# Optimization experiments

Measured on AMD Instinct MI355X. Metric: run time of the kernel, lower is better.

## Reference

```python
import jax, jax.numpy as jnp
import numpy as np

NUM_GROUPS = 32
EPS = 1e-6


def group_norm(x, gamma, beta):
    # x: [B, C, H, W]
    b, c, h, w = x.shape
    xg = x.reshape(b, NUM_GROUPS, c // NUM_GROUPS, h, w)
    mean = xg.mean(axis=(2, 3, 4), keepdims=True)
    var = xg.var(axis=(2, 3, 4), keepdims=True)
    xn = ((xg - mean) * jax.lax.rsqrt(var + EPS)).reshape(b, c, h, w)
    return xn * gamma[None, :, None, None] + beta[None, :, None, None]


def setup_inputs() -> dict:
    key = jax.random.key(0)
    ks = jax.random.split(key, 10)
    B, C, H, W = 2, 512, 64, 64
    s = 1.0 / np.sqrt(C)
    return {
        "x": jax.random.normal(ks[0], (B, C, H, W), dtype=jnp.float32),
        "gamma": jnp.ones((C,), jnp.float32),
        "beta": jnp.zeros((C,), jnp.float32),
        "Wq": jax.random.normal(ks[1], (C, C), jnp.float32) * s,
        "bq": jnp.zeros((C,), jnp.float32),
        "Wk": jax.random.normal(ks[2], (C, C), jnp.float32) * s,
        "bk": jnp.zeros((C,), jnp.float32),
        "Wv": jax.random.normal(ks[3], (C, C), jnp.float32) * s,
        "bv": jnp.zeros((C,), jnp.float32),
        "Wo": jax.random.normal(ks[4], (C, C), jnp.float32) * s,
        "bo": jnp.zeros((C,), jnp.float32),
    }


def reference(x, gamma, beta, Wq, bq, Wk, bk, Wv, bv, Wo, bo):
    b, c, h, w = x.shape
    hn = group_norm(x, gamma, beta)               # [B,C,H,W]
    hf = hn.reshape(b, c, h * w)                  # [B,C,N]
    # 1x1 convs == channel matmuls
    q = jnp.einsum('oc,bcn->bon', Wq, hf) + bq[None, :, None]
    k = jnp.einsum('oc,bcn->bon', Wk, hf) + bk[None, :, None]
    v = jnp.einsum('oc,bcn->bon', Wv, hf) + bv[None, :, None]
    scale = float(c) ** -0.5
    scores = jnp.einsum('bci,bcj->bij', q, k) * scale   # [B,N,N]
    attn = jax.nn.softmax(scores, axis=-1)
    out = jnp.einsum('bij,bcj->bci', attn, v)            # [B,C,N]
    out = jnp.einsum('oc,bcn->bon', Wo, out) + bo[None, :, None]
    return x + out.reshape(b, c, h, w)
```

## Files before the change

### kernel.cpp

```cpp
#include <hip/hip_runtime.h>

#define BB 2
#define CC 512
#define NS 4096
#define NGROUP 32
#define TILE 128
#define RSTRIDE 132

typedef __bf16 bf16_8 __attribute__((ext_vector_type(8)));
typedef __bf16 bf16_4 __attribute__((ext_vector_type(4)));
typedef float f32_4 __attribute__((ext_vector_type(4)));

#define SMEM_BYTES 65536
#define SMEM256 131072

__device__ __forceinline__ void gld_lds16(const __bf16* g, __bf16* l) {
  __builtin_amdgcn_global_load_lds(
      (const __attribute__((address_space(1))) unsigned int*)g,
      (__attribute__((address_space(3))) unsigned int*)l, 16, 0, 0);
}

__global__ __launch_bounds__(256) void prep(const float* __restrict__ w0, const float* __restrict__ w1,
                                            const float* __restrict__ w2, const float* __restrict__ w3,
                                            __bf16* __restrict__ o0, __bf16* __restrict__ o1,
                                            __bf16* __restrict__ o2, __bf16* __restrict__ o3,
                                            const float* __restrict__ x,
                                            float* __restrict__ st) {
  const int bid = blockIdx.x;
  if (bid >= 1024) {
    const int idx = bid - 1024;
    const int g = idx >> 2;
    const int ch = idx & 3;
    const float4* p = (const float4*)(x + (size_t)g * 65536 + (size_t)ch * 16384);
    float s = 0.f, q = 0.f;
    for (int i = threadIdx.x; i < 4096; i += 256) {
      float4 v = p[i];
      s += v.x + v.y + v.z + v.w;
      q += v.x * v.x + v.y * v.y + v.z * v.z + v.w * v.w;
    }
#pragma unroll
    for (int off = 32; off > 0; off >>= 1) {
      s += __shfl_down(s, off, 64);
      q += __shfl_down(q, off, 64);
    }
    __shared__ float ls[4], lq[4];
    int wave = threadIdx.x >> 6, lane = threadIdx.x & 63;
    if (lane == 0) { ls[wave] = s; lq[wave] = q; }
    __syncthreads();
    if (threadIdx.x == 0) {
      st[g * 8 + ch * 2 + 0] = ls[0] + ls[1] + ls[2] + ls[3];
      st[g * 8 + ch * 2 + 1] = lq[0] + lq[1] + lq[2] + lq[3];
    }
    return;
  }
  int tsel = bid >> 8;
  int i = (bid & 255) * 256 + threadIdx.x;
  const float* src = tsel == 0 ? w0 : tsel == 1 ? w1 : tsel == 2 ? w2 : w3;
  __bf16* dst = tsel == 0 ? o0 : tsel == 1 ? o1 : tsel == 2 ? o2 : o3;
  float4 v = ((const float4*)src)[i];
  bf16_4 r;
  r[0] = (__bf16)v.x; r[1] = (__bf16)v.y; r[2] = (__bf16)v.z; r[3] = (__bf16)v.w;
  ((bf16_4*)dst)[i] = r;
}

__global__ __launch_bounds__(256) void gn_apply_t(const float* __restrict__ x,
                                                  const float* __restrict__ st,
                                                  const float* __restrict__ gamma,
                                                  const float* __restrict__ beta,
                                                  __bf16* __restrict__ hnT) {
  __shared__ float tile[32][33];
  int b = blockIdx.z;
  int c0 = blockIdx.y * 32;
  int n0 = blockIdx.x * 32;
  int tx = threadIdx.x;
  int ty = threadIdx.y;
  const float* xb = x + (size_t)b * CC * NS;
#pragma unroll
  for (int i = 0; i < 4; i++) {
    int c = c0 + ty + i * 8;
    int g8 = (b * NGROUP + (c >> 4)) * 8;
    float S = st[g8 + 0] + st[g8 + 2] + st[g8 + 4] + st[g8 + 6];
    float Q = st[g8 + 1] + st[g8 + 3] + st[g8 + 5] + st[g8 + 7];
    float mean = S * (1.f / 65536.f);
    float var = Q * (1.f / 65536.f) - mean * mean;
    float rstd = rsqrtf(var + 1e-6f);
    float v = xb[(size_t)c * NS + n0 + tx];
    tile[ty + i * 8][tx] = (v - mean) * rstd * gamma[c] + beta[c];
  }
  __syncthreads();
  __bf16* out = hnT + (size_t)b * NS * CC;
#pragma unroll
  for (int i = 0; i < 4; i++) {
    int n = n0 + ty + i * 8;
    out[(size_t)n * CC + c0 + tx] = (__bf16)tile[tx][ty + i * 8];
  }
}

__device__ __forceinline__ void gemm_core8(const __bf16* __restrict__ A, const __bf16* __restrict__ B,
                                           int K, int lda, int ldb,
                                           __bf16* lds, f32_4 (&acc)[4][2]) {
  const int t = threadIdx.x;
  const int lane = t & 63;
  const int wave = t >> 6;
  const int lrow = lane & 15, quad = lane >> 4;
  const int wrow = (wave >> 2) * 64, wcol = (wave & 3) * 32;
  const int co = (quad ^ ((lrow >> 1) & 3)) * 8;
  const int r0 = t >> 2;
  const int kp = ((t & 3) ^ ((t >> 3) & 3)) * 8;
  const __bf16* pA = A + (size_t)r0 * lda + kp;
  const __bf16* pB = B + (size_t)r0 * ldb + kp;
  {
    __bf16* lA = lds;
    __bf16* lB = lds + 8192;
    gld_lds16(pA,      &lA[t * 8]);
    gld_lds16(pA + 32, &lA[4096 + t * 8]);
    gld_lds16(pB,      &lB[t * 8]);
    gld_lds16(pB + 32, &lB[4096 + t * 8]);
  }
  int buf = 0;
  for (int k0 = 0; k0 < K; k0 += 64, buf ^= 1) {
    __syncthreads();
    if (k0 + 64 < K) {
      __bf16* lA = lds + (buf ^ 1) * 16384;
      __bf16* lB = lA + 8192;
      gld_lds16(pA + k0 + 64, &lA[t * 8]);
      gld_lds16(pA + k0 + 96, &lA[4096 + t * 8]);
      gld_lds16(pB + k0 + 64, &lB[t * 8]);
      gld_lds16(pB + k0 + 96, &lB[4096 + t * 8]);
    }
    const __bf16* bA = lds + buf * 16384;
    const __bf16* bB = bA + 8192;
#pragma unroll
    for (int ks = 0; ks < 2; ks++) {
      const __bf16* la = bA + ks * 4096;
      const __bf16* lb = bB + ks * 4096;
      bf16_8 af[4], bfr[2];
#pragma unroll
      for (int i = 0; i < 4; i++)
        af[i] = *(const bf16_8*)&la[(wrow + i * 16 + lrow) * 32 + co];
#pragma unroll
      for (int j = 0; j < 2; j++)
        bfr[j] = *(const bf16_8*)&lb[(wcol + j * 16 + lrow) * 32 + co];
#pragma unroll
      for (int i = 0; i < 4; i++)
#pragma unroll
        for (int j = 0; j < 2; j++)
          acc[i][j] = __builtin_amdgcn_mfma_f32_16x16x32_bf16(af[i], bfr[j], acc[i][j], 0, 0, 0);
    }
  }
}

__device__ __forceinline__ void stage_acc8(float* ls, const f32_4 (&acc)[4][2], int pass) {
  const int t = threadIdx.x;
  const int lane = t & 63, wave = t >> 6;
  const int lrow = lane & 15, quad = lane >> 4;
  const int wrow = (wave >> 2) * 64, wcol = (wave & 3) * 32;
  if ((wrow >> 6) == pass) {
#pragma unroll
    for (int i = 0; i < 4; i++)
#pragma unroll
      for (int r = 0; r < 4; r++)
#pragma unroll
        for (int jj = 0; jj < 2; jj++)
          ls[(i * 16 + quad * 4 + r) * RSTRIDE + wcol + jj * 16 + lrow] = acc[i][jj][r];
  }
}

__device__ __forceinline__ void drain_bf16_8(const float* ls, __bf16* gdst, int ldg) {
  const int t = threadIdx.x;
#pragma unroll
  for (int k2 = 0; k2 < 4; k2++) {
    int idx = k2 * 512 + t;
    int row = idx >> 5, col = (idx & 31) * 4;
    f32_4 v = *(const f32_4*)&ls[row * RSTRIDE + col];
    bf16_4 o;
    o[0] = (__bf16)v[0]; o[1] = (__bf16)v[1]; o[2] = (__bf16)v[2]; o[3] = (__bf16)v[3];
    *(bf16_4*)&gdst[(size_t)row * ldg + col] = o;
  }
}

__device__ __forceinline__ void gemm_core256(const __bf16* __restrict__ A,
                                             const __bf16* __restrict__ B,
                                             int K, int lda, int ldb,
                                             __bf16* lds, f32_4 (&acc)[8][4]) {
  const int t = threadIdx.x;
  const int lane = t & 63;
  const int wave = t >> 6;
  const int lrow = lane & 15, quad = lane >> 4;
  const int wm = wave >> 2, wn = wave & 3;
  const int r0 = t >> 2;
  const int kp = ((t & 3) ^ ((t >> 3) & 3)) * 8;
  const __bf16* gA0 = A + (size_t)r0 * lda + kp;
  const __bf16* gA1 = A + (size_t)(r0 + 128) * lda + kp;
  const __bf16* gB0 = B + (size_t)r0 * ldb + kp;
  const __bf16* gB1 = B + (size_t)(r0 + 128) * ldb + kp;
  const int co = (quad ^ ((lrow >> 1) & 3)) * 8;
  const int aoff = (wm * 128 + lrow) * 32 + co;
  const int boff = 16384 + (wn * 64 + lrow) * 32 + co;
  const int KT = K >> 6;

#define STG(bufv, isB, srcp, hh, ktv)                                         \
  {                                                                           \
    __bf16* d_ = lds + (bufv) * 32768 + (isB) * 16384 + (hh) * 4096 + t * 8;  \
    const __bf16* s_ = (srcp) + (ktv) * 64;                                   \
    gld_lds16(s_, d_);                                                        \
    gld_lds16(s_ + 32, d_ + 8192);                                            \
  }
#define LOAD_AF(IH)                                                           \
  _Pragma("unroll") for (int i = 0; i < 4; i++)                               \
      _Pragma("unroll") for (int ks = 0; ks < 2; ks++)                        \
          af[i][ks] = *(const bf16_8*)&bb[aoff + ((IH) * 4 + i) * 512 + ks * 8192];
#define LOAD_BV(J0)                                                           \
  _Pragma("unroll") for (int j = 0; j < 2; j++)                               \
      _Pragma("unroll") for (int ks = 0; ks < 2; ks++)                        \
          bv[(J0) + j][ks] = *(const bf16_8*)&bb[boff + ((J0) + j) * 512 + ks * 8192];
#define MFMA16(I0, J0)                                                        \
  _Pragma("unroll") for (int ks = 0; ks < 2; ks++)                            \
      _Pragma("unroll") for (int i = 0; i < 4; i++)                           \
          _Pragma("unroll") for (int j = 0; j < 2; j++)                       \
              acc[(I0) + i][(J0) + j] = __builtin_amdgcn_mfma_f32_16x16x32_bf16( \
                  af[i][ks], bv[(J0) + j][ks], acc[(I0) + i][(J0) + j], 0, 0, 0);
#define PHASE_BEGIN()                                                         \
  __builtin_amdgcn_s_barrier();                                               \
  asm volatile("s_waitcnt lgkmcnt(0)" ::: "memory");                          \
  __builtin_amdgcn_sched_barrier(0);                                          \
  __builtin_amdgcn_s_setprio(1);
#define PHASE_END()                                                           \
  __builtin_amdgcn_s_setprio(0);                                              \
  __builtin_amdgcn_s_barrier();

  STG(0, 0, gA0, 0, 0)
  STG(0, 0, gA1, 1, 0)
  STG(0, 1, gB0, 0, 0)
  STG(0, 1, gB1, 1, 0)
  STG(1, 1, gB0, 0, 1)
  STG(1, 1, gB1, 1, 1)
  asm volatile("s_waitcnt vmcnt(4)" ::: "memory");
  __builtin_amdgcn_s_barrier();

  for (int it = 0; it < (KT >> 1); ++it) {
#pragma unroll
    for (int h = 0; h < 2; ++h) {
      const int kt = 2 * it + h;
      const __bf16* bb = lds + h * 32768;
      bf16_8 af[4][2], bv[4][2];
      LOAD_AF(0)
      LOAD_BV(0)
      if (kt + 1 < KT) STG(h ^ 1, 0, gA0, 0, kt + 1)
      PHASE_BEGIN()
      MFMA16(0, 0)
      PHASE_END()
      LOAD_BV(2)
      if (kt + 1 < KT) STG(h ^ 1, 0, gA1, 1, kt + 1)
      PHASE_BEGIN()
      MFMA16(0, 2)
      PHASE_END()
      LOAD_AF(1)
      if (kt + 2 < KT) STG(h, 1, gB0, 0, kt + 2)
      PHASE_BEGIN()
      MFMA16(4, 0)
      PHASE_END()
      if (kt + 2 < KT) STG(h, 1, gB1, 1, kt + 2)
      PHASE_BEGIN()
      MFMA16(4, 2)
      __builtin_amdgcn_s_setprio(0);
      if (kt + 2 < KT) {
        asm volatile("s_waitcnt vmcnt(4)" ::: "memory");
      } else {
        asm volatile("s_waitcnt vmcnt(0)" ::: "memory");
      }
      __builtin_amdgcn_s_barrier();
    }
  }
#undef STG
#undef LOAD_AF
#undef LOAD_BV
#undef MFMA16
#undef PHASE_BEGIN
#undef PHASE_END
}

__device__ __forceinline__ void gemm_coreF(const __bf16* __restrict__ A,
                                           const __bf16* __restrict__ B,
                                           int K, int lda, int ldb,
                                           __bf16* lds, f32_4 (&acc)[8][4]) {
  const int t = threadIdx.x;
  const int lane = t & 63;
  const int wave = t >> 6;
  const int lrow = lane & 15, quad = lane >> 4;
  const int wm = wave >> 2, wn = wave & 3;
  const int r0 = t >> 2;
  const int kp = ((t & 3) ^ ((t >> 3) & 3)) * 8;
  const __bf16* gA0 = A + (size_t)r0 * lda + kp;
  const __bf16* gA1 = A + (size_t)(r0 + 128) * lda + kp;
  const __bf16* gB0 = B + (size_t)r0 * ldb + kp;
  const __bf16* gB1 = B + (size_t)(r0 + 128) * ldb + kp;
  const int co = (quad ^ ((lrow >> 1) & 3)) * 8;
  const int aoff = (wm * 128 + lrow) * 32 + co;
  const int boff = 16384 + (wn * 64 + lrow) * 32 + co;
  const int KT = K >> 6;

  {
    __bf16* d = lds + t * 8;
    gld_lds16(gA0,      d);
    gld_lds16(gA1,      d + 4096);
    gld_lds16(gA0 + 32, d + 8192);
    gld_lds16(gA1 + 32, d + 12288);
    gld_lds16(gB0,      d + 16384);
    gld_lds16(gB1,      d + 20480);
    gld_lds16(gB0 + 32, d + 24576);
    gld_lds16(gB1 + 32, d + 28672);
  }
  int buf = 0;
  for (int kt = 0; kt < KT; ++kt, buf ^= 1) {
    __syncthreads();
    if (kt + 1 < KT) {
      __bf16* d = lds + (buf ^ 1) * 32768 + t * 8;
      const int go = (kt + 1) * 64;
      gld_lds16(gA0 + go,      d);
      gld_lds16(gA1 + go,      d + 4096);
      gld_lds16(gA0 + go + 32, d + 8192);
      gld_lds16(gA1 + go + 32, d + 12288);
      gld_lds16(gB0 + go,      d + 16384);
      gld_lds16(gB1 + go,      d + 20480);
      gld_lds16(gB0 + go + 32, d + 24576);
      gld_lds16(gB1 + go + 32, d + 28672);
    }
    const __bf16* bb = lds + buf * 32768;
#pragma unroll
    for (int ks = 0; ks < 2; ks++) {
      bf16_8 af[8], bv[4];
#pragma unroll
      for (int f = 0; f < 8; f++)
        af[f] = *(const bf16_8*)&bb[aoff + f * 512 + ks * 8192];
#pragma unroll
      for (int j = 0; j < 4; j++)
        bv[j] = *(const bf16_8*)&bb[boff + j * 512 + ks * 8192];
#pragma unroll
      for (int f = 0; f < 8; f++)
#pragma unroll
        for (int j = 0; j < 4; j++)
          acc[f][j] = __builtin_amdgcn_mfma_f32_16x16x32_bf16(af[f], bv[j], acc[f][j], 0, 0, 0);
    }
  }
}

__global__ __launch_bounds__(512, 2) void e_gemm256(const __bf16* __restrict__ qT,
                                                    const __bf16* __restrict__ kT,
                                                    __bf16* __restrict__ E,
                                                    float* __restrict__ l,
                                                    float scale) {
  extern __shared__ __bf16 ldsdyn[];
  const int bid = blockIdx.x;
  const int lin = (bid & 7) * 64 + (bid >> 3);
  const int b = lin >> 8;
  const int rm = lin & 255;
  const int R = rm >> 5, s = rm & 31;
  const int mt = (R >> 2) * 8 + (s >> 2);
  const int nt = (R & 3) * 4 + (s & 3);
  const int m0 = mt * 256, n0 = nt * 256;
  const long long sBNC = (long long)NS * CC;
  const long long sBNN = (long long)NS * NS;
  const __bf16* Ap = qT + (size_t)b * sBNC + (size_t)m0 * CC;
  const __bf16* Bp = kT + (size_t)b * sBNC + (size_t)n0 * CC;

  f32_4 acc[8][4];
#pragma unroll
  for (int i = 0; i < 8; i++)
#pragma unroll
    for (int j = 0; j < 4; j++) acc[i][j] = {0.f, 0.f, 0.f, 0.f};

  gemm_coreF(Ap, Bp, CC, CC, CC, ldsdyn, acc);

  const int t = threadIdx.x;
  const int lane = t & 63, wave = t >> 6;
  const int lrow = lane & 15, quad = lane >> 4;
  const int wm = wave >> 2, wn = wave & 3;
  __bf16* Ep = E + (size_t)b * sBNN;
  float* lp = l + (size_t)b * NS;
#pragma unroll
  for (int i = 0; i < 8; i++) {
#pragma unroll
    for (int r = 0; r < 4; r++) {
      int gm = m0 + wm * 128 + i * 16 + quad * 4 + r;
      float rp = 0.f;
#pragma unroll
      for (int j = 0; j < 4; j++) {
        int gn = n0 + wn * 64 + j * 16 + lrow;
        float ev = __expf(acc[i][j][r] * scale);
        rp += ev;
        Ep[(size_t)gm * NS + gn] = (__bf16)ev;
      }
      rp += __shfl_down(rp, 8, 16);
      rp += __shfl_down(rp, 4, 16);
      rp += __shfl_down(rp, 2, 16);
      rp += __shfl_down(rp, 1, 16);
      if (lrow == 0) atomicAdd(&lp[gm], rp);
    }
  }
}

__global__ __launch_bounds__(512, 2) void ao256(const __bf16* __restrict__ E,
                                                const __bf16* __restrict__ vv,
                                                __bf16* __restrict__ p0,
                                                __bf16* __restrict__ p1,
                                                __bf16* __restrict__ p2,
                                                __bf16* __restrict__ p3) {
  extern __shared__ __bf16 ldsdyn[];
  const int bid = blockIdx.x;
  const int lin = (bid & 7) * 32 + (bid >> 3);
  const int split = lin >> 6;
  const int rem = lin & 63;
  const int b = rem >> 5;
  const int mt = (rem & 31) >> 1;
  const int nt = rem & 1;
  const int m0 = mt * 256, n0 = nt * 256;
  const long long sBNN = (long long)NS * NS;
  const long long sBCN = (long long)CC * NS;
  const long long sBNC = (long long)NS * CC;
  const __bf16* Ap = E + (size_t)b * sBNN + (size_t)m0 * NS + (size_t)split * 1024;
  const __bf16* Bp = vv + (size_t)b * sBCN + (size_t)n0 * NS + (size_t)split * 1024;
  __bf16* Cp = (split == 0 ? p0 : split == 1 ? p1 : split == 2 ? p2 : p3) + (size_t)b * sBNC;

  f32_4 acc[8][4];
#pragma unroll
  for (int i = 0; i < 8; i++)
#pragma unroll
    for (int j = 0; j < 4; j++) acc[i][j] = {0.f, 0.f, 0.f, 0.f};

  gemm_core256(Ap, Bp, 1024, NS, NS, ldsdyn, acc);

  const int t = threadIdx.x;
  const int lane = t & 63, wave = t >> 6;
  const int lrow = lane & 15, quad = lane >> 4;
  const int wm = wave >> 2, wn = wave & 3;
#pragma unroll
  for (int i = 0; i < 8; i++) {
#pragma unroll
    for (int r = 0; r < 4; r++) {
      int gm = m0 + wm * 128 + i * 16 + quad * 4 + r;
#pragma unroll
      for (int j = 0; j < 4; j++) {
        int gn = n0 + wn * 64 + j * 16 + lrow;
        Cp[(size_t)gm * CC + gn] = (__bf16)acc[i][j][r];
      }
    }
  }
}

__global__ __launch_bounds__(512, 4) void qkv_gemm(const __bf16* __restrict__ hnT,
                                                   const __bf16* __restrict__ Wq,
                                                   const __bf16* __restrict__ Wk,
                                                   const __bf16* __restrict__ Wv,
                                                   const float* __restrict__ bq,
                                                   const float* __restrict__ bk,
                                                   const float* __restrict__ bv,
                                                   __bf16* __restrict__ qT,
                                                   __bf16* __restrict__ kT,
                                                   __bf16* __restrict__ vv) {
  __shared__ char smem[SMEM_BYTES];
  __bf16* lds = (__bf16*)smem;
  float* lsr = (float*)smem;
  const int b = blockIdx.z;
  const int id = blockIdx.x;
  const int sel = id >> 7;
  const int r = id & 127;
  const long long sBNC = (long long)NS * CC;
  const long long sBCN = (long long)CC * NS;

  int m0, n0, N;
  const __bf16 *Ap, *Bp;
  __bf16* Cp;
  const float* bias;
  if (sel < 2) {
    m0 = (r >> 2) * TILE;
    n0 = (r & 3) * TILE;
    Ap = hnT + (size_t)b * sBNC + (size_t)m0 * CC;
    Bp = (sel == 0 ? Wq : Wk) + (size_t)n0 * CC;
    Cp = (sel == 0 ? qT : kT) + (size_t)b * sBNC;
    bias = (sel == 0 ? bq : bk);
    N = CC;
  } else {
    m0 = (r & 3) * TILE;
    n0 = (r >> 2) * TILE;
    Ap = Wv + (size_t)m0 * CC;
    Bp = hnT + (size_t)b * sBNC + (size_t)n0 * CC;
    Cp = vv + (size_t)b * sBCN;
    bias = bv;
    N = NS;
  }

  f32_4 acc[4][2];
#pragma unroll
  for (int i = 0; i < 4; i++)
#pragma unroll
    for (int j = 0; j < 2; j++) acc[i][j] = {0.f, 0.f, 0.f, 0.f};

  gemm_core8(Ap, Bp, CC, CC, CC, lds, acc);

  const int t = threadIdx.x;
  const int lane = t & 63;
  const int lrow = lane & 15, quad = lane >> 4;
  const int wave = t >> 6;
  const int wrow = (wave >> 2) * 64, wcol = (wave & 3) * 32;
#pragma unroll
  for (int i = 0; i < 4; i++)
#pragma unroll
    for (int r2 = 0; r2 < 4; r2++) {
      float rowb = (sel == 2) ? bias[m0 + wrow + i * 16 + quad * 4 + r2] : 0.f;
#pragma unroll
      for (int j = 0; j < 2; j++) {
        float cb = (sel < 2) ? bias[n0 + wcol + j * 16 + lrow] : rowb;
        acc[i][j][r2] += cb;
      }
    }

#pragma unroll
  for (int p = 0; p < 2; p++) {
    __syncthreads();
    stage_acc8(lsr, acc, p);
    __syncthreads();
    drain_bf16_8(lsr, Cp + (size_t)(m0 + p * 64) * N + n0, N);
  }
}

__global__ __launch_bounds__(256) void reduce_ao4(const __bf16* __restrict__ p0,
                                                  const __bf16* __restrict__ p1,
                                                  const __bf16* __restrict__ p2,
                                                  const __bf16* __restrict__ p3,
                                                  const float* __restrict__ l,
                                                  __bf16* __restrict__ o) {
  int i = blockIdx.x * 256 + threadIdx.x;
  int row = i >> 6;
  float inv = 1.f / l[row];
  bf16_8 a = ((const bf16_8*)p0)[i];
  bf16_8 c = ((const bf16_8*)p1)[i];
  bf16_8 d = ((const bf16_8*)p2)[i];
  bf16_8 e = ((const bf16_8*)p3)[i];
  bf16_8 r;
#pragma unroll
  for (int k = 0; k < 8; k++)
    r[k] = (__bf16)(((float)a[k] + (float)c[k] + (float)d[k] + (float)e[k]) * inv);
  ((bf16_8*)o)[i] = r;
}

__global__ __launch_bounds__(512, 4) void wo_fused(const __bf16* __restrict__ Wo,
                                                   const __bf16* __restrict__ aoT,
                                                   const float* __restrict__ bo,
                                                   const float* __restrict__ x,
                                                   float* __restrict__ out) {
  __shared__ char smem[SMEM_BYTES];
  __bf16* lds = (__bf16*)smem;
  float* lsr = (float*)smem;
  const int b = blockIdx.z;
  const int m0 = blockIdx.y * TILE;
  const int n0 = blockIdx.x * TILE;
  const long long sBNC = (long long)NS * CC;
  const long long sBCN = (long long)CC * NS;
  const __bf16* Ap = Wo + (size_t)m0 * CC;
  const __bf16* Bp = aoT + (size_t)b * sBNC + (size_t)n0 * CC;
  const float* xb = x + (size_t)b * sBCN;
  float* ob = out + (size_t)b * sBCN;

  f32_4 acc[4][2];
#pragma unroll
  for (int i = 0; i < 4; i++)
#pragma unroll
    for (int j = 0; j < 2; j++) acc[i][j] = {0.f, 0.f, 0.f, 0.f};

  gemm_core8(Ap, Bp, CC, CC, CC, lds, acc);

  const int t = threadIdx.x;
#pragma unroll
  for (int p = 0; p < 2; p++) {
    __syncthreads();
    stage_acc8(lsr, acc, p);
    __syncthreads();
#pragma unroll
    for (int k2 = 0; k2 < 4; k2++) {
      int idx = k2 * 512 + t;
      int row = idx >> 5, col = (idx & 31) * 4;
      int o = m0 + p * 64 + row;
      f32_4 v = *(const f32_4*)&lsr[row * RSTRIDE + col];
      float bias = bo[o];
      float4 xr = *(const float4*)&xb[(size_t)o * NS + n0 + col];
      float4 rr;
      rr.x = v[0] + bias + xr.x;
      rr.y = v[1] + bias + xr.y;
      rr.z = v[2] + bias + xr.z;
      rr.w = v[3] + bias + xr.w;
      *(float4*)&ob[(size_t)o * NS + n0 + col] = rr;
    }
  }
}

extern "C" void kernel_launch(void* const* d_in, const int* in_sizes, int n_in,
                              void* d_out, int out_size, void* d_ws, size_t ws_size,
                              hipStream_t stream) {
  const float* x = (const float*)d_in[0];
  const float* gamma = (const float*)d_in[1];
  const float* beta = (const float*)d_in[2];
  const float* Wq = (const float*)d_in[3];
  const float* bq = (const float*)d_in[4];
  const float* Wk = (const float*)d_in[5];
  const float* bk = (const float*)d_in[6];
  const float* Wv = (const float*)d_in[7];
  const float* bv = (const float*)d_in[8];
  const float* Wo = (const float*)d_in[9];
  const float* bo = (const float*)d_in[10];
  float* out = (float*)d_out;

  char* ws = (char*)d_ws;
  __bf16* hnT = (__bf16*)(ws + 0);
  __bf16* qT  = (__bf16*)(ws + 8388608);
  __bf16* kT  = (__bf16*)(ws + 16777216);
  __bf16* vv  = (__bf16*)(ws + 25165824);
  __bf16* aoT = (__bf16*)(ws + 33554432);
  __bf16* Eb  = (__bf16*)(ws + 41943040);
  __bf16* Wqb = (__bf16*)(ws + 109051904);
  __bf16* Wkb = (__bf16*)(ws + 109576192);
  __bf16* Wvb = (__bf16*)(ws + 110100480);
  __bf16* Wob = (__bf16*)(ws + 110624768);
  float* stats = (float*)(ws + 111149056);
  float* lsum = (float*)(ws + 109051904);
  __bf16* p0 = hnT;
  __bf16* p1 = qT;
  __bf16* p2 = kT;
  __bf16* p3 = aoT;

  const float scale = 0.044194173824159216f;

  static int smem_attr_set = 0;
  if (!smem_attr_set) {
    hipFuncSetAttribute(reinterpret_cast<const void*>(e_gemm256),
                        hipFuncAttributeMaxDynamicSharedMemorySize, SMEM256);
    hipFuncSetAttribute(reinterpret_cast<const void*>(ao256),
                        hipFuncAttributeMaxDynamicSharedMemorySize, SMEM256);
    smem_attr_set = 1;
  }

  prep<<<1024 + 4 * BB * NGROUP, 256, 0, stream>>>(Wq, Wk, Wv, Wo, Wqb, Wkb, Wvb, Wob, x, stats);
  gn_apply_t<<<dim3(NS / 32, CC / 32, BB), dim3(32, 8), 0, stream>>>(x, stats, gamma, beta, hnT);

  qkv_gemm<<<dim3(384, 1, BB), 512, 0, stream>>>(hnT, Wqb, Wkb, Wvb, bq, bk, bv, qT, kT, vv);

  hipMemsetAsync(lsum, 0, BB * NS * sizeof(float), stream);
  e_gemm256<<<512, 512, SMEM256, stream>>>(qT, kT, Eb, lsum, scale);

  ao256<<<256, 512, SMEM256, stream>>>(Eb, vv, p0, p1, p2, p3);
  reduce_ao4<<<2048, 256, 0, stream>>>(p0, p1, p2, p3, lsum, aoT);

  wo_fused<<<dim3(NS / TILE, CC / TILE, BB), 512, 0, stream>>>(Wob, aoT, bo, x, out);
}
```

Baseline: 223.2 us.

## Replace split-K attention-value GEMM and reduce kernel with full-K 128-tile kernel

The E·V GEMM was previously split four ways along K using 256x256 tiles, wrote bf16 partials and then ran a separate reduce kernel that summed them and applied the softmax normalization. It now runs one full-K pass per 128x128 tile (256 blocks, static 64KB LDS, higher occupancy) and applies the 1/l normalization in the epilogue. This removes the partial-sum writes, their reread and an extra launch. In exchange each block runs a much longer K loop with smaller tiles, so operand reuse per block is lower.

```diff
diff --git a/kernel.cpp b/kernel.cpp
--- a/kernel.cpp
+++ b/kernel.cpp
@@ -177,107 +177,6 @@
     o[0] = (__bf16)v[0]; o[1] = (__bf16)v[1]; o[2] = (__bf16)v[2]; o[3] = (__bf16)v[3];
     *(bf16_4*)&gdst[(size_t)row * ldg + col] = o;
   }
-}
-
-__device__ __forceinline__ void gemm_core256(const __bf16* __restrict__ A,
-                                             const __bf16* __restrict__ B,
-                                             int K, int lda, int ldb,
-                                             __bf16* lds, f32_4 (&acc)[8][4]) {
-  const int t = threadIdx.x;
-  const int lane = t & 63;
-  const int wave = t >> 6;
-  const int lrow = lane & 15, quad = lane >> 4;
-  const int wm = wave >> 2, wn = wave & 3;
-  const int r0 = t >> 2;
-  const int kp = ((t & 3) ^ ((t >> 3) & 3)) * 8;
-  const __bf16* gA0 = A + (size_t)r0 * lda + kp;
-  const __bf16* gA1 = A + (size_t)(r0 + 128) * lda + kp;
-  const __bf16* gB0 = B + (size_t)r0 * ldb + kp;
-  const __bf16* gB1 = B + (size_t)(r0 + 128) * ldb + kp;
-  const int co = (quad ^ ((lrow >> 1) & 3)) * 8;
-  const int aoff = (wm * 128 + lrow) * 32 + co;
-  const int boff = 16384 + (wn * 64 + lrow) * 32 + co;
-  const int KT = K >> 6;
-
-#define STG(bufv, isB, srcp, hh, ktv)                                         \
-  {                                                                           \
-    __bf16* d_ = lds + (bufv) * 32768 + (isB) * 16384 + (hh) * 4096 + t * 8;  \
-    const __bf16* s_ = (srcp) + (ktv) * 64;                                   \
-    gld_lds16(s_, d_);                                                        \
-    gld_lds16(s_ + 32, d_ + 8192);                                            \
-  }
-#define LOAD_AF(IH)                                                           \
-  _Pragma("unroll") for (int i = 0; i < 4; i++)                               \
-      _Pragma("unroll") for (int ks = 0; ks < 2; ks++)                        \
-          af[i][ks] = *(const bf16_8*)&bb[aoff + ((IH) * 4 + i) * 512 + ks * 8192];
-#define LOAD_BV(J0)                                                           \
-  _Pragma("unroll") for (int j = 0; j < 2; j++)                               \
-      _Pragma("unroll") for (int ks = 0; ks < 2; ks++)                        \
-          bv[(J0) + j][ks] = *(const bf16_8*)&bb[boff + ((J0) + j) * 512 + ks * 8192];
-#define MFMA16(I0, J0)                                                        \
-  _Pragma("unroll") for (int ks = 0; ks < 2; ks++)                            \
-      _Pragma("unroll") for (int i = 0; i < 4; i++)                           \
-          _Pragma("unroll") for (int j = 0; j < 2; j++)                       \
-              acc[(I0) + i][(J0) + j] = __builtin_amdgcn_mfma_f32_16x16x32_bf16( \
-                  af[i][ks], bv[(J0) + j][ks], acc[(I0) + i][(J0) + j], 0, 0, 0);
-#define PHASE_BEGIN()                                                         \
-  __builtin_amdgcn_s_barrier();                                               \
-  asm volatile("s_waitcnt lgkmcnt(0)" ::: "memory");                          \
-  __builtin_amdgcn_sched_barrier(0);                                          \
-  __builtin_amdgcn_s_setprio(1);
-#define PHASE_END()                                                           \
-  __builtin_amdgcn_s_setprio(0);                                              \
-  __builtin_amdgcn_s_barrier();
-
-  STG(0, 0, gA0, 0, 0)
-  STG(0, 0, gA1, 1, 0)
-  STG(0, 1, gB0, 0, 0)
-  STG(0, 1, gB1, 1, 0)
-  STG(1, 1, gB0, 0, 1)
-  STG(1, 1, gB1, 1, 1)
-  asm volatile("s_waitcnt vmcnt(4)" ::: "memory");
-  __builtin_amdgcn_s_barrier();
-
-  for (int it = 0; it < (KT >> 1); ++it) {
-#pragma unroll
-    for (int h = 0; h < 2; ++h) {
-      const int kt = 2 * it + h;
-      const __bf16* bb = lds + h * 32768;
-      bf16_8 af[4][2], bv[4][2];
-      LOAD_AF(0)
-      LOAD_BV(0)
-      if (kt + 1 < KT) STG(h ^ 1, 0, gA0, 0, kt + 1)
-      PHASE_BEGIN()
-      MFMA16(0, 0)
-      PHASE_END()
-      LOAD_BV(2)
-      if (kt + 1 < KT) STG(h ^ 1, 0, gA1, 1, kt + 1)
-      PHASE_BEGIN()
-      MFMA16(0, 2)
-      PHASE_END()
-      LOAD_AF(1)
-      if (kt + 2 < KT) STG(h, 1, gB0, 0, kt + 2)
-      PHASE_BEGIN()
-      MFMA16(4, 0)
-      PHASE_END()
-      if (kt + 2 < KT) STG(h, 1, gB1, 1, kt + 2)
-      PHASE_BEGIN()
-      MFMA16(4, 2)
-      __builtin_amdgcn_s_setprio(0);
-      if (kt + 2 < KT) {
-        asm volatile("s_waitcnt vmcnt(4)" ::: "memory");
-      } else {
-        asm volatile("s_waitcnt vmcnt(0)" ::: "memory");
-      }
-      __builtin_amdgcn_s_barrier();
-    }
-  }
-#undef STG
-#undef LOAD_AF
-#undef LOAD_BV
-#undef MFMA16
-#undef PHASE_BEGIN
-#undef PHASE_END
 }
 
 __device__ __forceinline__ void gemm_coreF(const __bf16* __restrict__ A,
@@ -400,50 +299,53 @@
   }
 }
 
-__global__ __launch_bounds__(512, 2) void ao256(const __bf16* __restrict__ E,
-                                                const __bf16* __restrict__ vv,
-                                                __bf16* __restrict__ p0,
-                                                __bf16* __restrict__ p1,
-                                                __bf16* __restrict__ p2,
-                                                __bf16* __restrict__ p3) {
-  extern __shared__ __bf16 ldsdyn[];
+__global__ __launch_bounds__(512, 4) void ao_full(const __bf16* __restrict__ E,
+                                                  const __bf16* __restrict__ vv,
+                                                  const float* __restrict__ l,
+                                                  __bf16* __restrict__ aoT) {
+  __shared__ char smem[SMEM_BYTES];
+  __bf16* lds = (__bf16*)smem;
+  float* lsr = (float*)smem;
   const int bid = blockIdx.x;
   const int lin = (bid & 7) * 32 + (bid >> 3);
-  const int split = lin >> 6;
-  const int rem = lin & 63;
-  const int b = rem >> 5;
-  const int mt = (rem & 31) >> 1;
-  const int nt = rem & 1;
-  const int m0 = mt * 256, n0 = nt * 256;
+  const int b = lin >> 7;
+  const int rm = lin & 127;
+  const int mt = rm >> 2;
+  const int nt = rm & 3;
+  const int m0 = mt * TILE, n0 = nt * TILE;
   const long long sBNN = (long long)NS * NS;
   const long long sBCN = (long long)CC * NS;
   const long long sBNC = (long long)NS * CC;
-  const __bf16* Ap = E + (size_t)b * sBNN + (size_t)m0 * NS + (size_t)split * 1024;
-  const __bf16* Bp = vv + (size_t)b * sBCN + (size_t)n0 * NS + (size_t)split * 1024;
-  __bf16* Cp = (split == 0 ? p0 : split == 1 ? p1 : split == 2 ? p2 : p3) + (size_t)b * sBNC;
-
-  f32_4 acc[8][4];
-#pragma unroll
-  for (int i = 0; i < 8; i++)
-#pragma unroll
-    for (int j = 0; j < 4; j++) acc[i][j] = {0.f, 0.f, 0.f, 0.f};
-
-  gemm_core256(Ap, Bp, 1024, NS, NS, ldsdyn, acc);
-
-  const int t = threadIdx.x;
-  const int lane = t & 63, wave = t >> 6;
-  const int lrow = lane & 15, quad = lane >> 4;
-  const int wm = wave >> 2, wn = wave & 3;
-#pragma unroll
-  for (int i = 0; i < 8; i++) {
-#pragma unroll
-    for (int r = 0; r < 4; r++) {
-      int gm = m0 + wm * 128 + i * 16 + quad * 4 + r;
-#pragma unroll
-      for (int j = 0; j < 4; j++) {
-        int gn = n0 + wn * 64 + j * 16 + lrow;
-        Cp[(size_t)gm * CC + gn] = (__bf16)acc[i][j][r];
-      }
+  const __bf16* Ap = E + (size_t)b * sBNN + (size_t)m0 * NS;
+  const __bf16* Bp = vv + (size_t)b * sBCN + (size_t)n0 * NS;
+  const float* lp = l + (size_t)b * NS;
+  __bf16* Cp = aoT + (size_t)b * sBNC;
+
+  f32_4 acc[4][2];
+#pragma unroll
+  for (int i = 0; i < 4; i++)
+#pragma unroll
+    for (int j = 0; j < 2; j++) acc[i][j] = {0.f, 0.f, 0.f, 0.f};
+
+  gemm_core8(Ap, Bp, NS, NS, NS, lds, acc);
+
+  const int t = threadIdx.x;
+#pragma unroll
+  for (int p = 0; p < 2; p++) {
+    __syncthreads();
+    stage_acc8(lsr, acc, p);
+    __syncthreads();
+#pragma unroll
+    for (int k2 = 0; k2 < 4; k2++) {
+      int idx = k2 * 512 + t;
+      int row = idx >> 5, col = (idx & 31) * 4;
+      int gm = m0 + p * 64 + row;
+      float inv = 1.f / lp[gm];
+      f32_4 v = *(const f32_4*)&lsr[row * RSTRIDE + col];
+      bf16_4 o;
+      o[0] = (__bf16)(v[0] * inv); o[1] = (__bf16)(v[1] * inv);
+      o[2] = (__bf16)(v[2] * inv); o[3] = (__bf16)(v[3] * inv);
+      *(bf16_4*)&Cp[(size_t)gm * CC + n0 + col] = o;
     }
   }
 }
@@ -524,26 +426,6 @@
   }
 }
 
-__global__ __launch_bounds__(256) void reduce_ao4(const __bf16* __restrict__ p0,
-                                                  const __bf16* __restrict__ p1,
-                                                  const __bf16* __restrict__ p2,
-                                                  const __bf16* __restrict__ p3,
-                                                  const float* __restrict__ l,
-                                                  __bf16* __restrict__ o) {
-  int i = blockIdx.x * 256 + threadIdx.x;
-  int row = i >> 6;
-  float inv = 1.f / l[row];
-  bf16_8 a = ((const bf16_8*)p0)[i];
-  bf16_8 c = ((const bf16_8*)p1)[i];
-  bf16_8 d = ((const bf16_8*)p2)[i];
-  bf16_8 e = ((const bf16_8*)p3)[i];
-  bf16_8 r;
-#pragma unroll
-  for (int k = 0; k < 8; k++)
-    r[k] = (__bf16)(((float)a[k] + (float)c[k] + (float)d[k] + (float)e[k]) * inv);
-  ((bf16_8*)o)[i] = r;
-}
-
 __global__ __launch_bounds__(512, 4) void wo_fused(const __bf16* __restrict__ Wo,
                                                    const __bf16* __restrict__ aoT,
                                                    const float* __restrict__ bo,
@@ -623,10 +505,6 @@
   __bf16* Wob = (__bf16*)(ws + 110624768);
   float* stats = (float*)(ws + 111149056);
   float* lsum = (float*)(ws + 109051904);
-  __bf16* p0 = hnT;
-  __bf16* p1 = qT;
-  __bf16* p2 = kT;
-  __bf16* p3 = aoT;
 
   const float scale = 0.044194173824159216f;
 
@@ -634,8 +512,6 @@
   if (!smem_attr_set) {
     hipFuncSetAttribute(reinterpret_cast<const void*>(e_gemm256),
                         hipFuncAttributeMaxDynamicSharedMemorySize, SMEM256);
-    hipFuncSetAttribute(reinterpret_cast<const void*>(ao256),
-                        hipFuncAttributeMaxDynamicSharedMemorySize, SMEM256);
     smem_attr_set = 1;
   }
 
@@ -647,8 +523,7 @@
   hipMemsetAsync(lsum, 0, BB * NS * sizeof(float), stream);
   e_gemm256<<<512, 512, SMEM256, stream>>>(qT, kT, Eb, lsum, scale);
 
-  ao256<<<256, 512, SMEM256, stream>>>(Eb, vv, p0, p1, p2, p3);
-  reduce_ao4<<<2048, 256, 0, stream>>>(p0, p1, p2, p3, lsum, aoT);
+  ao_full<<<256, 512, 0, stream>>>(Eb, vv, lsum, aoT);
 
   wo_fused<<<dim3(NS / TILE, CC / TILE, BB), 512, 0, stream>>>(Wob, aoT, bo, x, out);
 }
```

New measurement: 229.8 us. 3.0% more time.
